# Kernel optimization log

Hardware: AMD Instinct MI355X
Metric: run time of the kernel (lower is better)

The kernel has to match this reference:

```python
import jax, jax.numpy as jnp
import numpy as np

B, S, H, E, K, DFF = 4, 2048, 1024, 8, 2, 4096


def setup_inputs() -> dict:
    key = jax.random.key(0)
    k0, k1, k2, k3 = jax.random.split(key, 4)
    sc = 0.02
    return {
        "x": jax.random.normal(k0, (B, S, H), jnp.float32),
        "gate_W": jax.random.normal(k1, (H, E), jnp.float32) * sc,
        "gate_b": jnp.zeros((E,), jnp.float32),
        "W1": jax.random.normal(k2, (H, DFF), jnp.float32) * sc,
        "b1": jnp.zeros((DFF,), jnp.float32),
        "W2": jax.random.normal(k3, (DFF, H), jnp.float32) * sc,
        "b2": jnp.zeros((H,), jnp.float32),
    }


def reference(x, gate_W, gate_b, W1, b1, W2, b2):
    b, s, h = x.shape
    x_flat = x.reshape(-1, h)                      # [T, H]
    gate_scores = x_flat @ gate_W + gate_b         # [T, E]
    top_k_scores, top_k_idx = jax.lax.top_k(gate_scores, K)   # [T, K]
    top_k_w = jax.nn.softmax(top_k_scores, axis=-1)           # [T, K]

    # All experts share the same weights (ModuleList reuses one module), so
    # sum_i w_i * expert_i(x) == expert(x) * sum_i w_i. top_k indices are
    # unique per token, so the per-token combine weight is sum of top-k weights.
    hdd = jax.nn.gelu(x_flat @ W1 + b1, approximate=False)    # [T, DFF]
    y = hdd @ W2 + b2                                         # [T, H]
    tok_w = top_k_w.sum(axis=-1)                              # [T] (== 1.0)
    output = (y * tok_w[:, None]).reshape(b, s, h)

    expert_load = gate_scores.mean(axis=0)                    # [E]
    aux_loss = (expert_load ** 2).sum()
    exp_counts = jnp.zeros((E,), jnp.int32).at[top_k_idx.ravel()].add(1)
    return output, aux_loss, exp_counts
```

## Files before the change

kernel.cpp:

```cpp
#include <hip/hip_runtime.h>
#include <hip/hip_bf16.h>
#include <math.h>

#define Tn   8192
#define Hn   1024
#define En   8
#define DFFn 4096

typedef __attribute__((ext_vector_type(8))) short bf16x8;
typedef __attribute__((ext_vector_type(8))) unsigned short u16x8;
typedef __attribute__((ext_vector_type(4))) float f32x4;

static __device__ inline unsigned short f2bf(float f) {
    __hip_bfloat16 h = __float2bfloat16(f);
    return __builtin_bit_cast(unsigned short, h);
}

__global__ __launch_bounds__(256) void prep(
    const float* __restrict__ W1, unsigned short* __restrict__ W1t,
    const float* __restrict__ W2, unsigned short* __restrict__ W2t,
    const float* __restrict__ x, const float* __restrict__ gW,
    const float* __restrict__ gb, unsigned short* __restrict__ xbf,
    float* __restrict__ tokw, float* __restrict__ load_sum,
    int* __restrict__ counts)
{
    __shared__ float smem[8 * 1024 + En];
    __shared__ int   s_cnt[En];
    const int tid = threadIdx.x;
    const int id  = blockIdx.x;

    if (id < 512) {
        const float* src; unsigned short* dst; int SR, SC, tb;
        if (id < 256) { src = W1; dst = W1t; SR = Hn;   SC = DFFn; tb = id; }
        else          { src = W2; dst = W2t; SR = DFFn; SC = Hn;   tb = id - 256; }
        const int tcs = SC >> 7;
        const int tr  = tb / tcs, tc = tb - tr * tcs;
        const int r0  = tr << 7, c0 = tc << 7;
        unsigned short* tile = (unsigned short*)smem;

        #pragma unroll
        for (int i = 0; i < 16; ++i) {
            int idx = tid + i * 256;
            int r = idx >> 5, c4 = (idx & 31) << 2;
            float4 v = *(const float4*)(src + (size_t)(r0 + r) * SC + c0 + c4);
            int cs = c4 ^ (((r >> 3) & 7) << 2);
            ushort4 pk;
            pk.x = f2bf(v.x); pk.y = f2bf(v.y);
            pk.z = f2bf(v.z); pk.w = f2bf(v.w);
            *(ushort4*)(tile + r * 128 + cs) = pk;
        }
        __syncthreads();
        #pragma unroll
        for (int i = 0; i < 8; ++i) {
            int idx = tid + i * 256;
            int n = idx >> 4, kg = idx & 15, k0 = kg << 3;
            int s = (kg & 7) << 2;
            u16x8 o;
            #pragma unroll
            for (int j = 0; j < 8; ++j)
                o[j] = tile[(k0 + j) * 128 + (n ^ s)];
            *(u16x8*)(dst + (size_t)(c0 + n) * SR + r0 + k0) = o;
        }
        return;
    }

    const int gid = id - 512;
    float* gwt    = smem;
    float* s_load = smem + 8 * 1024;
    if (tid < En) { s_load[tid] = 0.f; s_cnt[tid] = 0; }
    #pragma unroll
    for (int i = 0; i < 32; ++i) {
        int f = tid + i * 256;
        gwt[(f & 7) * 1024 + (f >> 3)] = gW[f];
    }
    __syncthreads();

    const int lane = tid & 63;
    const int wv   = tid >> 6;

    for (int tok = gid * 4 + wv; tok < Tn; tok += 4096) {
        const float4* xr = (const float4*)(x + (size_t)tok * Hn);
        float acc[8] = {0.f,0.f,0.f,0.f,0.f,0.f,0.f,0.f};
        #pragma unroll
        for (int j = 0; j < Hn / 256; ++j) {
            int h4 = j * 64 + lane;
            float4 xv = xr[h4];
            ushort4 pk;
            pk.x = f2bf(xv.x); pk.y = f2bf(xv.y);
            pk.z = f2bf(xv.z); pk.w = f2bf(xv.w);
            ((ushort4*)xbf)[(size_t)tok * (Hn / 4) + h4] = pk;
            #pragma unroll
            for (int e = 0; e < 8; ++e) {
                const float4 w = *(const float4*)(gwt + e * 1024 + h4 * 4);
                acc[e] += xv.x * w.x + xv.y * w.y + xv.z * w.z + xv.w * w.w;
            }
        }
        #pragma unroll
        for (int e = 0; e < 8; ++e) {
            float v = acc[e];
            #pragma unroll
            for (int off = 32; off > 0; off >>= 1) v += __shfl_xor(v, off, 64);
            acc[e] = v + gb[e];
        }
        if (lane == 0) {
            #pragma unroll
            for (int e = 0; e < 8; ++e) atomicAdd(&s_load[e], acc[e]);
            int i1 = 0; float v1 = acc[0];
            #pragma unroll
            for (int e = 1; e < 8; ++e) if (acc[e] > v1) { v1 = acc[e]; i1 = e; }
            int i2 = -1; float v2 = -3.0e38f;
            #pragma unroll
            for (int e = 0; e < 8; ++e) if (e != i1 && acc[e] > v2) { v2 = acc[e]; i2 = e; }
            atomicAdd(&s_cnt[i1], 1);
            atomicAdd(&s_cnt[i2], 1);
            float e2 = __expf(v2 - v1);
            float t  = 1.0f + e2;
            tokw[tok] = 1.0f / t + e2 / t;
        }
    }
    __syncthreads();
    if (tid < En) {
        atomicAdd(&load_sum[tid], s_load[tid]);
        atomicAdd(&counts[tid],   s_cnt[tid]);
    }
}

static __device__ inline bf16x8 ldsfrag(const char* base, int row, int chunk) {
    return *(const bf16x8*)(base + row * 128 + (((chunk) ^ (row & 7)) << 4));
}

template<int BN, int WM, int WN, int EPI>
__global__ __launch_bounds__(512, 2) void gemm8(
    const __hip_bfloat16* __restrict__ A,
    const __hip_bfloat16* __restrict__ Bt,
    const float* __restrict__ bias,
    const float* __restrict__ tokw,
    void* __restrict__ C, int N, int K, int nx,
    const float* __restrict__ load_sum, const int* __restrict__ counts,
    float* __restrict__ out_tail, int nblk)
{
    constexpr int BM = 256;
    constexpr int MR = (BM / WM) / 16;
    constexpr int NR = (BN / WN) / 16;
    constexpr int AU = BM / 64;
    constexpr int BU = BN / 64;
    constexpr int ABYTES = BM * 64 * 2;
    constexpr int BBYTES = BN * 64 * 2;
    constexpr int TILEB  = ABYTES + BBYTES;

    extern __shared__ char lds[];

    const int tid = threadIdx.x;
    const int id  = blockIdx.x;

    if (EPI == 0 && id >= nblk) {
        if (tid == 0) {
            float aux = 0.f;
            #pragma unroll
            for (int e = 0; e < En; ++e) {
                float m = load_sum[e] * (1.0f / (float)Tn);
                aux += m * m;
            }
            out_tail[0] = aux;
            #pragma unroll
            for (int e = 0; e < En; ++e) out_tail[1 + e] = (float)counts[e];
        }
        return;
    }

    int wg = id;
    { int xcd = wg & 7, idx = wg >> 3; wg = xcd * (nblk >> 3) + idx; }
    const int by = wg / nx, bx = wg % nx;
    const int m0 = by * BM, n0 = bx * BN;

    const int lane = tid & 63;
    const int wid  = tid >> 6;
    const int wn   = wid % WN;
    const int wm   = wid / WN;
    const int wrow = wm * (BM / WM);
    const int wcol = wn * (BN / WN);
    const int fr   = lane & 15;
    const int fq   = lane >> 4;

    const int sr = tid >> 3;
    const int sc = (tid & 7) ^ (sr & 7);
    unsigned aOff[AU], bOff[BU];
    #pragma unroll
    for (int u = 0; u < AU; ++u)
        aOff[u] = (unsigned)((m0 + u * 64 + sr) * K + sc * 8);
    #pragma unroll
    for (int u = 0; u < BU; ++u)
        bOff[u] = (unsigned)((n0 + u * 64 + sr) * K + sc * 8);

#define STA(b, u, kt) __builtin_amdgcn_global_load_lds( \
    (const __attribute__((address_space(1))) void*)(A + aOff[u] + (unsigned)(kt) * 64u), \
    (__attribute__((address_space(3))) void*)(lds + (b) * TILEB + (u) * 8192 + tid * 16), 16, 0, 0)
#define STB(b, u, kt) __builtin_amdgcn_global_load_lds( \
    (const __attribute__((address_space(1))) void*)(Bt + bOff[u] + (unsigned)(kt) * 64u), \
    (__attribute__((address_space(3))) void*)(lds + (b) * TILEB + ABYTES + (u) * 8192 + tid * 16), 16, 0, 0)

#define SBAR do { \
    __builtin_amdgcn_sched_barrier(0); \
    __builtin_amdgcn_s_barrier(); \
    __builtin_amdgcn_sched_barrier(0); } while (0)
#define WAITL(n) do { \
    asm volatile("s_waitcnt lgkmcnt(" #n ")" ::: "memory"); \
    __builtin_amdgcn_sched_barrier(0); } while (0)
#define VMC(n) do { asm volatile("s_waitcnt vmcnt(" #n ")" ::: "memory"); \
    __builtin_amdgcn_sched_barrier(0); } while (0)
#define PRIO1 __builtin_amdgcn_s_setprio(1)
#define PRIO0 __builtin_amdgcn_s_setprio(0)

    const int KT = K >> 6;

    if constexpr (WM == 2) {
        bf16x8 af[4][2];
        bf16x8 bfr[4][2];
        f32x4  acc[8][4];
        const f32x4 zero = {0.f, 0.f, 0.f, 0.f};
        #pragma unroll
        for (int i = 0; i < 8; ++i)
            #pragma unroll
            for (int j = 0; j < 4; ++j) acc[i][j] = zero;

#define RD_A(b, half) do { _Pragma("unroll") \
    for (int m_ = 0; m_ < 4; ++m_) { _Pragma("unroll") \
        for (int ks_ = 0; ks_ < 2; ++ks_) \
            af[m_][ks_] = ldsfrag(lds + (b) * TILEB, \
                wrow + ((half) * 4 + m_) * 16 + fr, ks_ * 4 + fq); } } while (0)
#define RD_B(b, nn) do { _Pragma("unroll") \
    for (int ks_ = 0; ks_ < 2; ++ks_) \
        bfr[nn][ks_] = ldsfrag(lds + (b) * TILEB + ABYTES, \
            wcol + (nn) * 16 + fr, ks_ * 4 + fq); } while (0)
#define MFMAQ(hm, hn) do { \
    PRIO1; \
    _Pragma("unroll") \
    for (int m_ = 0; m_ < 4; ++m_) { _Pragma("unroll") \
        for (int n_ = 0; n_ < 2; ++n_) { _Pragma("unroll") \
            for (int ks_ = 0; ks_ < 2; ++ks_) \
                acc[(hm) * 4 + m_][(hn) * 2 + n_] = \
                    __builtin_amdgcn_mfma_f32_16x16x32_bf16( \
                        af[m_][ks_], bfr[(hn) * 2 + n_][ks_], \
                        acc[(hm) * 4 + m_][(hn) * 2 + n_], 0, 0, 0); } } \
    PRIO0; } while (0)

        STA(0,0,0); STA(0,1,0); STA(0,2,0); STA(0,3,0);
        STB(0,0,0); STB(0,1,0); STB(0,2,0); STB(0,3,0);
        STA(1,0,1); STA(1,2,1);
        STB(1,0,1); STB(1,1,1); STB(1,2,1); STB(1,3,1);
        VMC(6);
        __builtin_amdgcn_s_barrier();
        __builtin_amdgcn_sched_barrier(0);
        RD_B(0,0); RD_B(0,1);

        for (int i = 0; i < (KT >> 1); ++i) {
            const int t1 = 2 * i + 1;
            const int c2 = (2 * i + 2 < KT) ? 2 * i + 2 : KT - 1;
            const int c3 = (2 * i + 3 < KT) ? 2 * i + 3 : KT - 1;

            RD_A(0,0);
            RD_B(0,2); RD_B(0,3);
            STA(1,1,t1); STA(1,3,t1);
            SBAR; WAITL(4); MFMAQ(0,0); SBAR;
            STA(0,0,c2); STA(0,2,c2);
            SBAR; WAITL(0); MFMAQ(0,1); SBAR;
            RD_A(0,1);
            STB(0,0,c2); STB(0,1,c2);
            SBAR; WAITL(0); MFMAQ(1,0); VMC(4); SBAR;
            RD_B(1,0); RD_B(1,1);
            STB(0,2,c2); STB(0,3,c2);
            SBAR; WAITL(4); MFMAQ(1,1); SBAR;
            RD_A(1,0);
            RD_B(1,2); RD_B(1,3);
            STA(0,1,c2); STA(0,3,c2);
            SBAR; WAITL(4); MFMAQ(0,0); SBAR;
            STA(1,0,c3); STA(1,2,c3);
            SBAR; WAITL(0); MFMAQ(0,1); SBAR;
            RD_A(1,1);
            STB(1,0,c3); STB(1,1,c3);
            SBAR; WAITL(0); MFMAQ(1,0); VMC(4); SBAR;
            RD_B(0,0); RD_B(0,1);
            STB(1,2,c3); STB(1,3,c3);
            SBAR; WAITL(4); MFMAQ(1,1); SBAR;
        }

        float bias4[4];
        #pragma unroll
        for (int ni = 0; ni < 4; ++ni)
            bias4[ni] = bias[n0 + wcol + ni * 16 + fr];
        #pragma unroll
        for (int mi = 0; mi < 8; ++mi) {
            #pragma unroll
            for (int ni = 0; ni < 4; ++ni) {
                const int col = n0 + wcol + ni * 16 + fr;
                const int rb  = m0 + wrow + mi * 16 + fq * 4;
                #pragma unroll
                for (int i2 = 0; i2 < 4; ++i2) {
                    float u  = acc[mi][ni][i2] + bias4[ni];
                    float uu = u * u;
                    float z  = u * __fmaf_rn(uu, -0.07135607f, -1.59576912f);
                    float e  = __expf(z);
                    float g  = u * __builtin_amdgcn_rcpf(1.0f + e);
                    ((__hip_bfloat16*)C)[(size_t)(rb + i2) * N + col] =
                        __float2bfloat16(g);
                }
            }
        }
#undef RD_A
#undef RD_B
#undef MFMAQ
    } else {
        bf16x8 afh0[2][2], afh1[2][2];
        bf16x8 bfrS0[4][2], bfrS1[4][2];
        f32x4  acc[4][4];
        const f32x4 zero = {0.f, 0.f, 0.f, 0.f};
        #pragma unroll
        for (int i = 0; i < 4; ++i)
            #pragma unroll
            for (int j = 0; j < 4; ++j) acc[i][j] = zero;

#define RD_AH(dst, b, half) do { _Pragma("unroll") \
    for (int m_ = 0; m_ < 2; ++m_) { _Pragma("unroll") \
        for (int ks_ = 0; ks_ < 2; ++ks_) \
            dst[m_][ks_] = ldsfrag(lds + (b) * TILEB, \
                wrow + ((half) * 2 + m_) * 16 + fr, ks_ * 4 + fq); } } while (0)
#define RD_BS(dst, b) do { _Pragma("unroll") \
    for (int n_ = 0; n_ < 4; ++n_) { _Pragma("unroll") \
        for (int ks_ = 0; ks_ < 2; ++ks_) \
            dst[n_][ks_] = ldsfrag(lds + (b) * TILEB + ABYTES, \
                wcol + n_ * 16 + fr, ks_ * 4 + fq); } } while (0)
#define MFMAH(afx, bfx, hm) do { \
    PRIO1; \
    _Pragma("unroll") \
    for (int m_ = 0; m_ < 2; ++m_) { _Pragma("unroll") \
        for (int n_ = 0; n_ < 4; ++n_) { _Pragma("unroll") \
            for (int ks_ = 0; ks_ < 2; ++ks_) \
                acc[(hm) * 2 + m_][n_] = \
                    __builtin_amdgcn_mfma_f32_16x16x32_bf16( \
                        bfx[n_][ks_], afx[m_][ks_], \
                        acc[(hm) * 2 + m_][n_], 0, 0, 0); } } \
    PRIO0; } while (0)

        STA(0,0,0); STA(0,1,0); STA(0,2,0); STA(0,3,0);
        STB(0,0,0); STB(0,1,0);
        STB(1,0,1); STB(1,1,1);
        STA(1,0,1); STA(1,1,1); STA(1,2,1); STA(1,3,1);
        VMC(6);
        __builtin_amdgcn_s_barrier();
        __builtin_amdgcn_sched_barrier(0);
        RD_AH(afh0, 0, 0); RD_BS(bfrS0, 0);

        for (int i = 0; i < (KT >> 1); ++i) {
            const int c2 = (2 * i + 2 < KT) ? 2 * i + 2 : KT - 1;
            const int c3 = (2 * i + 3 < KT) ? 2 * i + 3 : KT - 1;

            RD_AH(afh1, 0, 1);
            SBAR; WAITL(0); MFMAH(afh0, bfrS0, 0); VMC(0); SBAR;
            RD_AH(afh0, 1, 0); RD_BS(bfrS1, 1);
            STB(0,0,c2); STB(0,1,c2);
            STA(0,0,c2); STA(0,1,c2); STA(0,2,c2); STA(0,3,c2);
            SBAR; WAITL(12); MFMAH(afh1, bfrS0, 1); SBAR;
            RD_AH(afh1, 1, 1);
            SBAR; WAITL(0); MFMAH(afh0, bfrS1, 0); VMC(0); SBAR;
            RD_AH(afh0, 0, 0); RD_BS(bfrS0, 0);
            STB(1,0,c3); STB(1,1,c3);
            STA(1,0,c3); STA(1,1,c3); STA(1,2,c3); STA(1,3,c3);
            SBAR; WAITL(12); MFMAH(afh1, bfrS1, 1); SBAR;
        }

        const int mrow0 = m0 + wrow + fr;
        const int ncol0 = n0 + wcol + fq * 4;
        float4 b4[4];
        #pragma unroll
        for (int ni = 0; ni < 4; ++ni)
            b4[ni] = *(const float4*)(bias + ncol0 + ni * 16);

        #pragma unroll
        for (int mi = 0; mi < 4; ++mi) {
            const int row = mrow0 + mi * 16;
            const float tw = tokw[row];
            #pragma unroll
            for (int ni = 0; ni < 4; ++ni) {
                f32x4 v = acc[mi][ni];
                float4 o;
                o.x = (v[0] + b4[ni].x) * tw;
                o.y = (v[1] + b4[ni].y) * tw;
                o.z = (v[2] + b4[ni].z) * tw;
                o.w = (v[3] + b4[ni].w) * tw;
                *(float4*)((float*)C + (size_t)row * N + ncol0 + ni * 16) = o;
            }
        }
#undef RD_AH
#undef RD_BS
#undef MFMAH
    }

#undef STA
#undef STB
#undef SBAR
#undef WAITL
#undef VMC
#undef PRIO1
#undef PRIO0
}

extern "C" void kernel_launch(void* const* d_in, const int* in_sizes, int n_in,
                              void* d_out, int out_size, void* d_ws, size_t ws_size,
                              hipStream_t stream)
{
    const float* x  = (const float*)d_in[0];
    const float* gW = (const float*)d_in[1];
    const float* gb = (const float*)d_in[2];
    const float* W1 = (const float*)d_in[3];
    const float* b1 = (const float*)d_in[4];
    const float* W2 = (const float*)d_in[5];
    const float* b2 = (const float*)d_in[6];
    float* out = (float*)d_out;

    char* ws = (char*)d_ws;
    __hip_bfloat16* xbf = (__hip_bfloat16*)ws;  ws += (size_t)Tn * Hn * 2;
    __hip_bfloat16* W1t = (__hip_bfloat16*)ws;  ws += (size_t)Hn * DFFn * 2;
    __hip_bfloat16* W2t = (__hip_bfloat16*)ws;  ws += (size_t)Hn * DFFn * 2;
    __hip_bfloat16* hdd = (__hip_bfloat16*)ws;  ws += (size_t)Tn * DFFn * 2;
    float* tokw     = (float*)ws;               ws += (size_t)Tn * 4;
    float* load_sum = (float*)ws;               ws += En * 4;
    int*   counts   = (int*)ws;                 ws += En * 4;

    static bool attr_done = false;
    if (!attr_done) {
        (void)hipFuncSetAttribute(
            reinterpret_cast<const void*>(&gemm8<256, 2, 4, 0>),
            hipFuncAttributeMaxDynamicSharedMemorySize, 131072);
        (void)hipFuncSetAttribute(
            reinterpret_cast<const void*>(&gemm8<128, 4, 2, 1>),
            hipFuncAttributeMaxDynamicSharedMemorySize, 98304);
        attr_done = true;
    }

    hipMemsetAsync(load_sum, 0, En * 4 * 2, stream);

    prep<<<1536, 256, 0, stream>>>(W1, (unsigned short*)W1t,
                                   W2, (unsigned short*)W2t,
                                   x, gW, gb, (unsigned short*)xbf,
                                   tokw, load_sum, counts);

    gemm8<256, 2, 4, 0><<<513, 512, 131072, stream>>>(
        xbf, W1t, b1, nullptr, hdd, DFFn, Hn, 16,
        load_sum, counts, out + (size_t)Tn * Hn, 512);

    gemm8<128, 4, 2, 1><<<256, 512, 98304, stream>>>(
        hdd, W2t, b2, tokw, out, Hn, DFFn, 8,
        nullptr, nullptr, nullptr, 256);
}
```

Before: 268.7 us.

## Double-buffer GEMM fragments, drop pre-MFMA barriers, and replace global atomics with per-block partials

In the first GEMM, the LDS fragment reads now go into alternating A/B register sets, so the next fragments load while the current MFMA group runs. This removes the leading barrier before each MFMA quarter and relaxes the lgkmcnt waits, at the cost of more VGPRs. The second GEMM's waits are relaxed from lgkmcnt(0) to lgkmcnt(4). The gating statistics are written as per-block partials and reduced in the tail block, which removes the memset and the global atomics. The extra registers could spill or lower occupancy, and the relaxed waits depend on the instruction counts being exact.

```diff
diff --git a/kernel.cpp b/kernel.cpp
--- a/kernel.cpp
+++ b/kernel.cpp
@@ -21,8 +21,8 @@
     const float* __restrict__ W2, unsigned short* __restrict__ W2t,
     const float* __restrict__ x, const float* __restrict__ gW,
     const float* __restrict__ gb, unsigned short* __restrict__ xbf,
-    float* __restrict__ tokw, float* __restrict__ load_sum,
-    int* __restrict__ counts)
+    float* __restrict__ tokw, float* __restrict__ pb_load,
+    int* __restrict__ pb_cnt)
 {
     __shared__ float smem[8 * 1024 + En];
     __shared__ int   s_cnt[En];
@@ -120,8 +120,8 @@
     }
     __syncthreads();
     if (tid < En) {
-        atomicAdd(&load_sum[tid], s_load[tid]);
-        atomicAdd(&counts[tid],   s_cnt[tid]);
+        pb_load[gid * En + tid] = s_load[tid];
+        pb_cnt [gid * En + tid] = s_cnt[tid];
     }
 }
 
@@ -136,7 +136,7 @@
     const float* __restrict__ bias,
     const float* __restrict__ tokw,
     void* __restrict__ C, int N, int K, int nx,
-    const float* __restrict__ load_sum, const int* __restrict__ counts,
+    const float* __restrict__ pb_load, const int* __restrict__ pb_cnt,
     float* __restrict__ out_tail, int nblk)
 {
     constexpr int BM = 256;
@@ -154,16 +154,29 @@
     const int id  = blockIdx.x;
 
     if (EPI == 0 && id >= nblk) {
+        float* sl = (float*)lds;
+        int*   sc = (int*)(lds + 64);
+        if (tid < En) { sl[tid] = 0.f; sc[tid] = 0; }
+        __syncthreads();
+        const int e = tid & 7;
+        float p = 0.f; int c = 0;
+        for (int g = tid >> 3; g < 1024; g += 64) {
+            p += pb_load[g * En + e];
+            c += pb_cnt [g * En + e];
+        }
+        atomicAdd(&sl[e], p);
+        atomicAdd(&sc[e], c);
+        __syncthreads();
         if (tid == 0) {
             float aux = 0.f;
             #pragma unroll
-            for (int e = 0; e < En; ++e) {
-                float m = load_sum[e] * (1.0f / (float)Tn);
+            for (int e2 = 0; e2 < En; ++e2) {
+                float m = sl[e2] * (1.0f / (float)Tn);
                 aux += m * m;
             }
             out_tail[0] = aux;
             #pragma unroll
-            for (int e = 0; e < En; ++e) out_tail[1 + e] = (float)counts[e];
+            for (int e2 = 0; e2 < En; ++e2) out_tail[1 + e2] = (float)sc[e2];
         }
         return;
     }
@@ -214,8 +227,9 @@
     const int KT = K >> 6;
 
     if constexpr (WM == 2) {
-        bf16x8 af[4][2];
-        bf16x8 bfr[4][2];
+        bf16x8 afX[4][2], afY[4][2];
+        bf16x8 bPa[2][2], bQa[2][2];
+        bf16x8 bPb[2][2], bQb[2][2];
         f32x4  acc[8][4];
         const f32x4 zero = {0.f, 0.f, 0.f, 0.f};
         #pragma unroll
@@ -223,16 +237,17 @@
             #pragma unroll
             for (int j = 0; j < 4; ++j) acc[i][j] = zero;
 
-#define RD_A(b, half) do { _Pragma("unroll") \
+#define RDAF(dst, b, half) do { _Pragma("unroll") \
     for (int m_ = 0; m_ < 4; ++m_) { _Pragma("unroll") \
         for (int ks_ = 0; ks_ < 2; ++ks_) \
-            af[m_][ks_] = ldsfrag(lds + (b) * TILEB, \
+            dst[m_][ks_] = ldsfrag(lds + (b) * TILEB, \
                 wrow + ((half) * 4 + m_) * 16 + fr, ks_ * 4 + fq); } } while (0)
-#define RD_B(b, nn) do { _Pragma("unroll") \
-    for (int ks_ = 0; ks_ < 2; ++ks_) \
-        bfr[nn][ks_] = ldsfrag(lds + (b) * TILEB + ABYTES, \
-            wcol + (nn) * 16 + fr, ks_ * 4 + fq); } while (0)
-#define MFMAQ(hm, hn) do { \
+#define RDBF(dst, b, pr) do { _Pragma("unroll") \
+    for (int n_ = 0; n_ < 2; ++n_) { _Pragma("unroll") \
+        for (int ks_ = 0; ks_ < 2; ++ks_) \
+            dst[n_][ks_] = ldsfrag(lds + (b) * TILEB + ABYTES, \
+                wcol + ((pr) * 2 + n_) * 16 + fr, ks_ * 4 + fq); } } while (0)
+#define MFMAQ(afb, bfb, hm, hn) do { \
     PRIO1; \
     _Pragma("unroll") \
     for (int m_ = 0; m_ < 4; ++m_) { _Pragma("unroll") \
@@ -240,7 +255,7 @@
             for (int ks_ = 0; ks_ < 2; ++ks_) \
                 acc[(hm) * 4 + m_][(hn) * 2 + n_] = \
                     __builtin_amdgcn_mfma_f32_16x16x32_bf16( \
-                        af[m_][ks_], bfr[(hn) * 2 + n_][ks_], \
+                        afb[m_][ks_], bfb[n_][ks_], \
                         acc[(hm) * 4 + m_][(hn) * 2 + n_], 0, 0, 0); } } \
     PRIO0; } while (0)
 
@@ -251,37 +266,37 @@
         VMC(6);
         __builtin_amdgcn_s_barrier();
         __builtin_amdgcn_sched_barrier(0);
-        RD_B(0,0); RD_B(0,1);
+        RDAF(afX, 0, 0); RDBF(bPa, 0, 0);
 
         for (int i = 0; i < (KT >> 1); ++i) {
             const int t1 = 2 * i + 1;
             const int c2 = (2 * i + 2 < KT) ? 2 * i + 2 : KT - 1;
             const int c3 = (2 * i + 3 < KT) ? 2 * i + 3 : KT - 1;
 
-            RD_A(0,0);
-            RD_B(0,2); RD_B(0,3);
+            RDBF(bQa, 0, 1);
             STA(1,1,t1); STA(1,3,t1);
-            SBAR; WAITL(4); MFMAQ(0,0); SBAR;
+            WAITL(4); MFMAQ(afX, bPa, 0, 0); SBAR;
+            RDAF(afY, 0, 1);
             STA(0,0,c2); STA(0,2,c2);
-            SBAR; WAITL(0); MFMAQ(0,1); SBAR;
-            RD_A(0,1);
+            WAITL(8); MFMAQ(afX, bQa, 0, 1); VMC(4); SBAR;
+            RDBF(bPb, 1, 0);
             STB(0,0,c2); STB(0,1,c2);
-            SBAR; WAITL(0); MFMAQ(1,0); VMC(4); SBAR;
-            RD_B(1,0); RD_B(1,1);
+            WAITL(4); MFMAQ(afY, bPa, 1, 0); SBAR;
+            RDAF(afX, 1, 0);
             STB(0,2,c2); STB(0,3,c2);
-            SBAR; WAITL(4); MFMAQ(1,1); SBAR;
-            RD_A(1,0);
-            RD_B(1,2); RD_B(1,3);
+            WAITL(8); MFMAQ(afY, bQa, 1, 1); VMC(4); SBAR;
+            RDBF(bQb, 1, 1);
             STA(0,1,c2); STA(0,3,c2);
-            SBAR; WAITL(4); MFMAQ(0,0); SBAR;
+            WAITL(4); MFMAQ(afX, bPb, 0, 0); SBAR;
+            RDAF(afY, 1, 1);
             STA(1,0,c3); STA(1,2,c3);
-            SBAR; WAITL(0); MFMAQ(0,1); SBAR;
-            RD_A(1,1);
+            WAITL(8); MFMAQ(afX, bQb, 0, 1); VMC(4); SBAR;
+            RDBF(bPa, 0, 0);
             STB(1,0,c3); STB(1,1,c3);
-            SBAR; WAITL(0); MFMAQ(1,0); VMC(4); SBAR;
-            RD_B(0,0); RD_B(0,1);
+            WAITL(4); MFMAQ(afY, bPb, 1, 0); SBAR;
+            RDAF(afX, 0, 0);
             STB(1,2,c3); STB(1,3,c3);
-            SBAR; WAITL(4); MFMAQ(1,1); SBAR;
+            WAITL(8); MFMAQ(afY, bQb, 1, 1); VMC(4); SBAR;
         }
 
         float bias4[4];
@@ -306,8 +321,8 @@
                 }
             }
         }
-#undef RD_A
-#undef RD_B
+#undef RDAF
+#undef RDBF
 #undef MFMAQ
     } else {
         bf16x8 afh0[2][2], afh1[2][2];
@@ -355,13 +370,13 @@
             const int c3 = (2 * i + 3 < KT) ? 2 * i + 3 : KT - 1;
 
             RD_AH(afh1, 0, 1);
-            SBAR; WAITL(0); MFMAH(afh0, bfrS0, 0); VMC(0); SBAR;
+            SBAR; WAITL(4); MFMAH(afh0, bfrS0, 0); VMC(0); SBAR;
             RD_AH(afh0, 1, 0); RD_BS(bfrS1, 1);
             STB(0,0,c2); STB(0,1,c2);
             STA(0,0,c2); STA(0,1,c2); STA(0,2,c2); STA(0,3,c2);
             SBAR; WAITL(12); MFMAH(afh1, bfrS0, 1); SBAR;
             RD_AH(afh1, 1, 1);
-            SBAR; WAITL(0); MFMAH(afh0, bfrS1, 0); VMC(0); SBAR;
+            SBAR; WAITL(4); MFMAH(afh0, bfrS1, 0); VMC(0); SBAR;
             RD_AH(afh0, 0, 0); RD_BS(bfrS0, 0);
             STB(1,0,c3); STB(1,1,c3);
             STA(1,0,c3); STA(1,1,c3); STA(1,2,c3); STA(1,3,c3);
@@ -423,8 +438,8 @@
     __hip_bfloat16* W2t = (__hip_bfloat16*)ws;  ws += (size_t)Hn * DFFn * 2;
     __hip_bfloat16* hdd = (__hip_bfloat16*)ws;  ws += (size_t)Tn * DFFn * 2;
     float* tokw     = (float*)ws;               ws += (size_t)Tn * 4;
-    float* load_sum = (float*)ws;               ws += En * 4;
-    int*   counts   = (int*)ws;                 ws += En * 4;
+    float* pb_load  = (float*)ws;               ws += 1024 * En * 4;
+    int*   pb_cnt   = (int*)ws;                 ws += 1024 * En * 4;
 
     static bool attr_done = false;
     if (!attr_done) {
@@ -437,16 +452,14 @@
         attr_done = true;
     }
 
-    hipMemsetAsync(load_sum, 0, En * 4 * 2, stream);
-
     prep<<<1536, 256, 0, stream>>>(W1, (unsigned short*)W1t,
                                    W2, (unsigned short*)W2t,
                                    x, gW, gb, (unsigned short*)xbf,
-                                   tokw, load_sum, counts);
+                                   tokw, pb_load, pb_cnt);
 
     gemm8<256, 2, 4, 0><<<513, 512, 131072, stream>>>(
         xbf, W1t, b1, nullptr, hdd, DFFn, Hn, 16,
-        load_sum, counts, out + (size_t)Tn * Hn, 512);
+        pb_load, pb_cnt, out + (size_t)Tn * Hn, 512);
 
     gemm8<128, 4, 2, 1><<<256, 512, 98304, stream>>>(
         hdd, W2t, b2, tokw, out, Hn, DFFn, 8,
```

After: 315.9 us. 17.5% more time.
